# Performance work log

Hardware: AMD Instinct MI355X
Metric: run time of the kernel (lower is better)

The kernel has to match this reference:

```python
import jax, jax.numpy as jnp
import numpy as np

B, H, W, C = 4, 64, 64, 128
C8 = C // 8  # query/key channels


def setup_inputs() -> dict:
    key = jax.random.key(0)
    ks = jax.random.split(key, 7)
    s_in = 1.0 / np.sqrt(C)
    x = jax.random.normal(ks[0], (B, H, W, C), dtype=jnp.float32)
    Wq = jax.random.normal(ks[1], (C, C8), dtype=jnp.float32) * s_in
    bq = jnp.zeros((C8,), dtype=jnp.float32)
    Wk = jax.random.normal(ks[2], (C, C8), dtype=jnp.float32) * s_in
    bk = jnp.zeros((C8,), dtype=jnp.float32)
    Wv = jax.random.normal(ks[3], (C, C), dtype=jnp.float32) * s_in
    bv = jnp.zeros((C,), dtype=jnp.float32)
    gamma = jnp.zeros((), dtype=jnp.float32)
    return {"x": x, "Wq": Wq, "bq": bq, "Wk": Wk, "bk": bk,
            "Wv": Wv, "bv": bv, "gamma": gamma}


def reference(x, Wq, bq, Wk, bk, Wv, bv, gamma):
    b, h, w, c = x.shape
    n = h * w
    xt = x.reshape(b, n, c)  # tokens
    # 1x1 convs == per-token linear projections
    q = xt @ Wq + bq          # [B, N, C/8]
    k = xt @ Wk + bk          # [B, N, C/8]
    v = xt @ Wv + bv          # [B, N, C]
    energy = jnp.einsum('bnd,bmd->bnm', q, k)   # [B, N, N]
    attention = jax.nn.softmax(energy, axis=-1)
    out = jnp.einsum('bnm,bmc->bnc', attention, v)  # [B, N, C]
    out = out.reshape(b, h, w, c)
    return out * gamma + x, attention
```

## Files before the change

kernel.cpp:

```cpp
#include <hip/hip_runtime.h>

#define B_   4
#define N_   4096
#define C_   128
#define C8_  16
#define BN_  (B_*N_)
#define SHIFT 8.0f
#define LOG2E 1.4426950408889634f

typedef _Float16 half4_t __attribute__((ext_vector_type(4)));
typedef float    f32x4   __attribute__((ext_vector_type(4)));

__global__ __launch_bounds__(256) void qkv_proj(
    const float* __restrict__ x,  const float* __restrict__ Wq,
    const float* __restrict__ bq, const float* __restrict__ Wk,
    const float* __restrict__ bk, const float* __restrict__ Wv,
    const float* __restrict__ bv, const float* __restrict__ gm,
    _Float16* __restrict__ q, _Float16* __restrict__ k,
    float* __restrict__ v, float* __restrict__ out)
{
    __shared__ float xs[16][132];
    const int tid = threadIdx.x;
    const int t0  = blockIdx.x * 16;

    {
        const int tt = tid >> 4, cs = (tid & 15) * 8;
        const float* src = x + (size_t)(t0 + tt) * C_ + cs;
        float4 a = *(const float4*)src;
        float4 b = *(const float4*)(src + 4);
        float* dst = out + (size_t)(t0 + tt) * C_ + cs;
        *(float4*)dst       = a;
        *(float4*)(dst + 4) = b;
        xs[tt][cs+0]=a.x; xs[tt][cs+1]=a.y; xs[tt][cs+2]=a.z; xs[tt][cs+3]=a.w;
        xs[tt][cs+4]=b.x; xs[tt][cs+5]=b.y; xs[tt][cs+6]=b.z; xs[tt][cs+7]=b.w;
    }
    __syncthreads();

    const int tt = tid >> 4;
    const int j  = tid & 15;

    float aq = bq[j], ak = bk[j];
    #pragma unroll 8
    for (int c = 0; c < C_; ++c) {
        float xv = xs[tt][c];
        aq = fmaf(xv, Wq[c*C8_ + j], aq);
        ak = fmaf(xv, Wk[c*C8_ + j], ak);
    }
    q[(size_t)(t0+tt)*C8_ + j] = (_Float16)(aq * LOG2E);
    k[(size_t)(t0+tt)*C8_ + j] = (_Float16)ak;

    if (gm[0] != 0.0f) {
        float av[8];
        #pragma unroll
        for (int u = 0; u < 8; ++u) av[u] = bv[j*8 + u];
        for (int c = 0; c < C_; ++c) {
            float xv = xs[tt][c];
            float4 w0 = *(const float4*)(Wv + (size_t)c*C_ + j*8);
            float4 w1 = *(const float4*)(Wv + (size_t)c*C_ + j*8 + 4);
            av[0]=fmaf(xv,w0.x,av[0]); av[1]=fmaf(xv,w0.y,av[1]);
            av[2]=fmaf(xv,w0.z,av[2]); av[3]=fmaf(xv,w0.w,av[3]);
            av[4]=fmaf(xv,w1.x,av[4]); av[5]=fmaf(xv,w1.y,av[5]);
            av[6]=fmaf(xv,w1.z,av[6]); av[7]=fmaf(xv,w1.w,av[7]);
        }
        float4* dst = (float4*)(v + (size_t)(t0+tt)*C_ + j*8);
        dst[0] = make_float4(av[0],av[1],av[2],av[3]);
        dst[1] = make_float4(av[4],av[5],av[6],av[7]);
    }
}

__global__ __launch_bounds__(256, 4) void attn_mfma(
    const _Float16* __restrict__ q, const _Float16* __restrict__ k,
    float* __restrict__ attn)
{
    __shared__ float lsum[4][16];
    const int tid  = threadIdx.x;
    const int bid  = (blockIdx.x & 7) * 128 + (blockIdx.x >> 3);
    const int b    = bid >> 8;
    const int row0 = (bid & 255) * 16;
    const int wave = tid >> 6, lane = tid & 63;
    const int rr   = lane & 15;
    const int g    = lane >> 4;

    const float ebase = -(SHIFT*LOG2E);

    const half4_t qb = *(const half4_t*)(q + (size_t)(b*N_ + row0 + rr)*C8_ + 4*g);

    const _Float16* kbase = k + (size_t)b*N_*C8_;
    const int col0 = wave * (N_/4);
    const int NT   = (N_/4)/16;
    const _Float16* kw = kbase + (size_t)(col0 + rr)*C8_ + 4*g;

    f32x4 acc4 = {0.f,0.f,0.f,0.f};
    {
        half4_t f0 = *(const half4_t*)(kw + (size_t)0*16*C8_);
        half4_t f1 = *(const half4_t*)(kw + (size_t)1*16*C8_);
        const f32x4 cin = {ebase, ebase, ebase, ebase};
        for (int s = 0; s < NT; ++s) {
            const int nn = (s+2 < NT) ? s+2 : s;
            half4_t f2 = *(const half4_t*)(kw + (size_t)nn*16*C8_);
            f32x4 d = __builtin_amdgcn_mfma_f32_16x16x16f16(f0, qb, cin, 0, 0, 0);
            acc4[0] += __builtin_amdgcn_exp2f(d[0]);
            acc4[1] += __builtin_amdgcn_exp2f(d[1]);
            acc4[2] += __builtin_amdgcn_exp2f(d[2]);
            acc4[3] += __builtin_amdgcn_exp2f(d[3]);
            f0 = f1; f1 = f2;
        }
    }
    float acc = (acc4[0]+acc4[1]) + (acc4[2]+acc4[3]);
    acc += __shfl_xor(acc, 16);
    acc += __shfl_xor(acc, 32);
    if (lane < 16) lsum[wave][lane] = acc;
    __syncthreads();
    const float tot = (lsum[0][rr] + lsum[1][rr]) + (lsum[2][rr] + lsum[3][rr]);
    const float cstv = ebase - __builtin_amdgcn_logf(tot);

    {
        float* adst = attn + (size_t)(b*N_ + row0 + rr)*N_ + col0 + 4*g;
        half4_t f0 = *(const half4_t*)(kw + (size_t)0*16*C8_);
        half4_t f1 = *(const half4_t*)(kw + (size_t)1*16*C8_);
        const f32x4 cin = {cstv, cstv, cstv, cstv};
        for (int s = 0; s < NT; ++s) {
            const int nn = (s+2 < NT) ? s+2 : s;
            half4_t f2 = *(const half4_t*)(kw + (size_t)nn*16*C8_);
            f32x4 d = __builtin_amdgcn_mfma_f32_16x16x16f16(f0, qb, cin, 0, 0, 0);
            f32x4 p;
            p[0] = __builtin_amdgcn_exp2f(d[0]);
            p[1] = __builtin_amdgcn_exp2f(d[1]);
            p[2] = __builtin_amdgcn_exp2f(d[2]);
            p[3] = __builtin_amdgcn_exp2f(d[3]);
            *(f32x4*)(adst + s*16) = p;
            f0 = f1; f1 = f2;
        }
    }
}

__global__ __launch_bounds__(256) void out_kernel(
    const float* __restrict__ x, const float* __restrict__ gm,
    const float* __restrict__ attn, const float* __restrict__ v,
    float* __restrict__ out)
{
    const float g = gm[0];
    if (g == 0.0f) return;
    __shared__ float sh[256];
    for (int rr = 0; rr < 8; ++rr) {
        const int row = blockIdx.x * 8 + rr;
        const int bb  = row >> 12;
        const int c   = threadIdx.x & 127;
        const int h   = threadIdx.x >> 7;
        const float* arow = attn + (size_t)row * N_;
        float acc = 0.f;
        for (int m = h*2048; m < (h+1)*2048; ++m)
            acc = fmaf(arow[m], v[(size_t)(bb*N_ + m)*C_ + c], acc);
        sh[threadIdx.x] = acc;
        __syncthreads();
        if (threadIdx.x < 128) {
            const float o = sh[threadIdx.x] + sh[threadIdx.x + 128];
            out[(size_t)row*C_ + c] = fmaf(g, o, x[(size_t)row*C_ + c]);
        }
        __syncthreads();
    }
}

extern "C" void kernel_launch(void* const* d_in, const int* in_sizes, int n_in,
                              void* d_out, int out_size, void* d_ws, size_t ws_size,
                              hipStream_t stream) {
    const float* x  = (const float*)d_in[0];
    const float* Wq = (const float*)d_in[1];
    const float* bq = (const float*)d_in[2];
    const float* Wk = (const float*)d_in[3];
    const float* bk = (const float*)d_in[4];
    const float* Wv = (const float*)d_in[5];
    const float* bv = (const float*)d_in[6];
    const float* gm = (const float*)d_in[7];

    float* out  = (float*)d_out;
    float* attn = out + (size_t)BN_ * C_;

    _Float16* q = (_Float16*)d_ws;
    _Float16* k = q + (size_t)BN_ * C8_;
    float*    v = (float*)(k + (size_t)BN_ * C8_);

    qkv_proj <<<BN_/16, 256, 0, stream>>>(x, Wq, bq, Wk, bk, Wv, bv, gm, q, k, v, out);
    attn_mfma<<<B_*(N_/16), 256, 0, stream>>>(q, k, attn);
    out_kernel<<<2048, 256, 0, stream>>>(x, gm, attn, v, out);
}
```

Before: 68.45 us.

## Fuse QKV projection into attention kernel with per-batch atomic grid barrier

Measured after the change: 214.7 us. 214% more time.

```diff
diff --git a/kernel.cpp b/kernel.cpp
--- a/kernel.cpp
+++ b/kernel.cpp
@@ -11,79 +11,89 @@
 typedef _Float16 half4_t __attribute__((ext_vector_type(4)));
 typedef float    f32x4   __attribute__((ext_vector_type(4)));
 
-__global__ __launch_bounds__(256) void qkv_proj(
+__global__ __launch_bounds__(256, 4) void fused_attn(
     const float* __restrict__ x,  const float* __restrict__ Wq,
     const float* __restrict__ bq, const float* __restrict__ Wk,
     const float* __restrict__ bk, const float* __restrict__ Wv,
     const float* __restrict__ bv, const float* __restrict__ gm,
-    _Float16* __restrict__ q, _Float16* __restrict__ k,
-    float* __restrict__ v, float* __restrict__ out)
+    _Float16* __restrict__ k, float* __restrict__ v,
+    int* __restrict__ cnt,
+    float* __restrict__ out, float* __restrict__ attn)
 {
     __shared__ float xs[16][132];
+    __shared__ _Float16 qs[16][16];
+    __shared__ float lsum[4][16];
+
     const int tid = threadIdx.x;
-    const int t0  = blockIdx.x * 16;
+    const int bid = blockIdx.x;
+    const int b   = bid >> 8;
+    const int r   = bid & 255;
+    const int t0  = b*N_ + r*16;
 
     {
         const int tt = tid >> 4, cs = (tid & 15) * 8;
         const float* src = x + (size_t)(t0 + tt) * C_ + cs;
-        float4 a = *(const float4*)src;
-        float4 b = *(const float4*)(src + 4);
+        float4 a  = *(const float4*)src;
+        float4 b4 = *(const float4*)(src + 4);
         float* dst = out + (size_t)(t0 + tt) * C_ + cs;
         *(float4*)dst       = a;
-        *(float4*)(dst + 4) = b;
-        xs[tt][cs+0]=a.x; xs[tt][cs+1]=a.y; xs[tt][cs+2]=a.z; xs[tt][cs+3]=a.w;
-        xs[tt][cs+4]=b.x; xs[tt][cs+5]=b.y; xs[tt][cs+6]=b.z; xs[tt][cs+7]=b.w;
+        *(float4*)(dst + 4) = b4;
+        xs[tt][cs+0]=a.x;  xs[tt][cs+1]=a.y;  xs[tt][cs+2]=a.z;  xs[tt][cs+3]=a.w;
+        xs[tt][cs+4]=b4.x; xs[tt][cs+5]=b4.y; xs[tt][cs+6]=b4.z; xs[tt][cs+7]=b4.w;
     }
     __syncthreads();
 
-    const int tt = tid >> 4;
-    const int j  = tid & 15;
-
-    float aq = bq[j], ak = bk[j];
-    #pragma unroll 8
-    for (int c = 0; c < C_; ++c) {
-        float xv = xs[tt][c];
-        aq = fmaf(xv, Wq[c*C8_ + j], aq);
-        ak = fmaf(xv, Wk[c*C8_ + j], ak);
-    }
-    q[(size_t)(t0+tt)*C8_ + j] = (_Float16)(aq * LOG2E);
-    k[(size_t)(t0+tt)*C8_ + j] = (_Float16)ak;
-
-    if (gm[0] != 0.0f) {
-        float av[8];
-        #pragma unroll
-        for (int u = 0; u < 8; ++u) av[u] = bv[j*8 + u];
+    {
+        const int tt = tid >> 4;
+        const int j  = tid & 15;
+        float aq = bq[j], ak = bk[j];
+        #pragma unroll 8
         for (int c = 0; c < C_; ++c) {
             float xv = xs[tt][c];
-            float4 w0 = *(const float4*)(Wv + (size_t)c*C_ + j*8);
-            float4 w1 = *(const float4*)(Wv + (size_t)c*C_ + j*8 + 4);
-            av[0]=fmaf(xv,w0.x,av[0]); av[1]=fmaf(xv,w0.y,av[1]);
-            av[2]=fmaf(xv,w0.z,av[2]); av[3]=fmaf(xv,w0.w,av[3]);
-            av[4]=fmaf(xv,w1.x,av[4]); av[5]=fmaf(xv,w1.y,av[5]);
-            av[6]=fmaf(xv,w1.z,av[6]); av[7]=fmaf(xv,w1.w,av[7]);
+            aq = fmaf(xv, Wq[c*C8_ + j], aq);
+            ak = fmaf(xv, Wk[c*C8_ + j], ak);
         }
-        float4* dst = (float4*)(v + (size_t)(t0+tt)*C_ + j*8);
-        dst[0] = make_float4(av[0],av[1],av[2],av[3]);
-        dst[1] = make_float4(av[4],av[5],av[6],av[7]);
+        qs[tt][j] = (_Float16)(aq * LOG2E);
+        k[(size_t)(t0+tt)*C8_ + j] = (_Float16)ak;
+
+        if (gm[0] != 0.0f) {
+            float av[8];
+            #pragma unroll
+            for (int u = 0; u < 8; ++u) av[u] = bv[j*8 + u];
+            for (int c = 0; c < C_; ++c) {
+                float xv = xs[tt][c];
+                float4 w0 = *(const float4*)(Wv + (size_t)c*C_ + j*8);
+                float4 w1 = *(const float4*)(Wv + (size_t)c*C_ + j*8 + 4);
+                av[0]=fmaf(xv,w0.x,av[0]); av[1]=fmaf(xv,w0.y,av[1]);
+                av[2]=fmaf(xv,w0.z,av[2]); av[3]=fmaf(xv,w0.w,av[3]);
+                av[4]=fmaf(xv,w1.x,av[4]); av[5]=fmaf(xv,w1.y,av[5]);
+                av[6]=fmaf(xv,w1.z,av[6]); av[7]=fmaf(xv,w1.w,av[7]);
+            }
+            float4* dst = (float4*)(v + (size_t)(t0+tt)*C_ + j*8);
+            dst[0] = make_float4(av[0],av[1],av[2],av[3]);
+            dst[1] = make_float4(av[4],av[5],av[6],av[7]);
+        }
     }
-}
+    __syncthreads();
 
-__global__ __launch_bounds__(256, 4) void attn_mfma(
-    const _Float16* __restrict__ q, const _Float16* __restrict__ k,
-    float* __restrict__ attn)
-{
-    __shared__ float lsum[4][16];
-    const int tid  = threadIdx.x;
-    const int bid  = (blockIdx.x & 7) * 128 + (blockIdx.x >> 3);
-    const int b    = bid >> 8;
-    const int row0 = (bid & 255) * 16;
+    if (tid == 0) {
+        __threadfence();
+        __hip_atomic_fetch_add(&cnt[b], 1, __ATOMIC_RELEASE,
+                               __HIP_MEMORY_SCOPE_AGENT);
+        while (__hip_atomic_load(&cnt[b], __ATOMIC_ACQUIRE,
+                                 __HIP_MEMORY_SCOPE_AGENT) < 256)
+            __builtin_amdgcn_s_sleep(4);
+        __threadfence();
+    }
+    __syncthreads();
+
     const int wave = tid >> 6, lane = tid & 63;
     const int rr   = lane & 15;
     const int g    = lane >> 4;
+    const int row0 = r * 16;
 
     const float ebase = -(SHIFT*LOG2E);
-
-    const half4_t qb = *(const half4_t*)(q + (size_t)(b*N_ + row0 + rr)*C8_ + 4*g);
+    const half4_t qb = *(const half4_t*)&qs[rr][4*g];
 
     const _Float16* kbase = k + (size_t)b*N_*C8_;
     const int col0 = wave * (N_/4);
@@ -111,7 +121,7 @@
     acc += __shfl_xor(acc, 32);
     if (lane < 16) lsum[wave][lane] = acc;
     __syncthreads();
-    const float tot = (lsum[0][rr] + lsum[1][rr]) + (lsum[2][rr] + lsum[3][rr]);
+    const float tot  = (lsum[0][rr] + lsum[1][rr]) + (lsum[2][rr] + lsum[3][rr]);
     const float cstv = ebase - __builtin_amdgcn_logf(tot);
 
     {
@@ -176,11 +186,12 @@
     float* out  = (float*)d_out;
     float* attn = out + (size_t)BN_ * C_;
 
-    _Float16* q = (_Float16*)d_ws;
-    _Float16* k = q + (size_t)BN_ * C8_;
-    float*    v = (float*)(k + (size_t)BN_ * C8_);
+    int*      cnt = (int*)d_ws;
+    _Float16* k   = (_Float16*)((char*)d_ws + 256);
+    float*    v   = (float*)(k + (size_t)BN_ * C8_);
 
-    qkv_proj <<<BN_/16, 256, 0, stream>>>(x, Wq, bq, Wk, bk, Wv, bv, gm, q, k, v, out);
-    attn_mfma<<<B_*(N_/16), 256, 0, stream>>>(q, k, attn);
+    hipMemsetAsync(d_ws, 0, 256, stream);
+    fused_attn<<<B_*(N_/16), 256, 0, stream>>>(x, Wq, bq, Wk, bk, Wv, bv, gm,
+                                               k, v, cnt, out, attn);
     out_kernel<<<2048, 256, 0, stream>>>(x, gm, attn, v, out);
 }
```
